# Optimization experiments

Measured on AMD Instinct MI355X. Metric: run time of the kernel, lower is better.

Reference implementation:

```python
import jax, jax.numpy as jnp
import numpy as np

N_ENT = 16384   # num_entities
N_REL = 50      # num relations
D = 128         # embedding dim
B = 4           # num bases
E = 262144      # num edges (avg degree 16)


def setup_inputs() -> dict:
    key = jax.random.key(0)
    k1, k2, k3, k4, k5, k6 = jax.random.split(key, 6)
    x = jax.random.normal(k1, (N_ENT, D), dtype=jnp.float32)
    bases = jax.random.normal(k2, (B, D, D), dtype=jnp.float32) * 0.05
    comps = jax.random.normal(k3, (N_REL, B), dtype=jnp.float32)
    alpha = jax.random.normal(k4, (N_REL, 1), dtype=jnp.float32)
    edge_index = jax.random.randint(k5, (2, E), 0, N_ENT, dtype=jnp.int64)
    edge_type = jax.random.randint(k6, (E,), 0, N_REL, dtype=jnp.int64)
    return {"x": x, "bases": bases, "comps": comps, "alpha": alpha,
            "edge_index": edge_index, "edge_type": edge_type}


def reference(x, bases, comps, alpha, edge_index, edge_type):
    # R-GCN basis-decomposition message passing:
    #   msg_e = (h_j @ W_{r(e)}) * alpha_{r(e)} * norm_e,  W_r = sum_b comps[r,b] * bases[b]
    #   out_i = sum_{e: row(e)=i} msg_e
    n = x.shape[0]
    row, col = edge_index[0], edge_index[1]

    # edge_norm = 1/sqrt(D_row) * 1/sqrt(D_col) with out-degree over rows
    ones = jnp.ones(row.shape, x.dtype)
    deg = jax.ops.segment_sum(ones, row, num_segments=n)
    deg_inv = jnp.where(deg > 0, jax.lax.rsqrt(jnp.maximum(deg, 1.0)), 0.0)
    norm = deg_inv[row] * deg_inv[col]               # [E]

    h_j = x[col]                                     # [E, D] gather
    c_e = comps[edge_type]                           # [E, B] gather
    # sum_b c[e,b] * (h_j[e] @ bases[b])  ==  einsum over (b,d)
    hj_b = c_e[:, :, None] * h_j[:, None, :]         # [E, B, D]
    msg = jnp.einsum('ebd,bdf->ef', hj_b, bases)     # [E, D] big GEMM
    msg = msg * alpha[edge_type] * norm[:, None]

    out = jax.ops.segment_sum(msg, row, num_segments=n)  # scatter-add to nodes
    return out
```

## Files before the change

kernel.cpp:

```cpp
#include <hip/hip_runtime.h>
#include <stdint.h>

#define NENT 16384
#define NREL 50
#define NE   262144
#define BSTR 64
#define ASTR 260
#define POISON 0xAAAAAAAAu

typedef __attribute__((ext_vector_type(8))) short short8;
typedef __attribute__((ext_vector_type(4))) float float4v;

__device__ __forceinline__ float bf2f(uint32_t u){ return __uint_as_float(u << 16); }
__device__ __forceinline__ uint32_t fpack(float a, float b){
  uint32_t ua = __float_as_uint(a), ub = __float_as_uint(b);
  ua = (ua + 0x7fffu + ((ua >> 16) & 1u)) >> 16;
  ub = (ub + 0x7fffu + ((ub >> 16) & 1u)) >> 16;
  return ua | (ub << 16);
}
__device__ __forceinline__ unsigned short f2bf(float a){
  uint32_t ua = __float_as_uint(a);
  return (unsigned short)((ua + 0x7fffu + ((ua >> 16) & 1u)) >> 16);
}
__device__ __forceinline__ float rdlane_f(float v, int j){
  return __uint_as_float((uint32_t)__builtin_amdgcn_readlane((int)__float_as_uint(v), j));
}

__global__ __launch_bounds__(256) void k_prep(
    const float* __restrict__ x, const float* __restrict__ W,
    const float* __restrict__ comps, const float* __restrict__ alpha,
    const int* __restrict__ eidx, const int* __restrict__ etype,
    uint32_t* __restrict__ deg, float* __restrict__ acomb,
    unsigned short* __restrict__ WTf, uint32_t* __restrict__ xbf,
    uint32_t* __restrict__ bucket)
{
  int gid = blockIdx.x * 256 + threadIdx.x;
  int row = eidx[gid], col = eidx[NE + gid], r = etype[gid];
  uint32_t pos = atomicAdd(&deg[row], 1u) - POISON;
  if (pos < BSTR) bucket[row * BSTR + pos] = (uint32_t)col | ((uint32_t)r << 14);

  const float4* xin = (const float4*)x + gid * 2;
  float4 p0 = xin[0], p1 = xin[1];
  uint32_t* xo = xbf + gid * 4;
  xo[0] = fpack(p0.x, p0.y); xo[1] = fpack(p0.z, p0.w);
  xo[2] = fpack(p1.x, p1.y); xo[3] = fpack(p1.z, p1.w);

  if (gid < 65536){
    int k = gid >> 7, c = gid & 127;
    int n = c >> 4, m = c & 15, kc = k >> 5, q = (k >> 3) & 3, jj = k & 7;
    WTf[(((n * 16 + kc) * 4 + q) * 16 + m) * 8 + jj] = f2bf(W[gid]);
  }
  if (gid < NREL * 4) acomb[gid] = alpha[gid >> 2] * comps[gid];
}

__global__ __launch_bounds__(256, 8) void k_fused(
    const uint32_t* __restrict__ xbf, const uint32_t* __restrict__ deg,
    const float* __restrict__ acomb, const uint32_t* __restrict__ bucket,
    const unsigned short* __restrict__ WTf, float* __restrict__ outf)
{
  __shared__ uint32_t A_lds[16 * ASTR];
  int t = threadIdx.x, lane = t & 63, wv = t >> 6;
  int row0 = blockIdx.x * 8;

  for (int rr = wv * 2; rr < wv * 2 + 2; ++rr){
    int i = row0 + rr;
    int d = (int)(deg[i] - POISON);
    uint32_t* Arow = &A_lds[rr * ASTR];
    if (d == 0){
      Arow[lane] = 0; Arow[lane+64] = 0; Arow[lane+128] = 0; Arow[lane+192] = 0;
      continue;
    }
    int de = min(d, BSTR);
    uint32_t rec = bucket[i * BSTR + min(lane, de - 1)];
    int colN = (int)(rec & 0x3FFFu);
    int colO = colN << 6;
    int rL   = (int)(rec >> 14);
    int dc   = (int)(deg[colN] - POISON);
    float dic = (dc > 0) ? rsqrtf((float)dc) : 0.f;
    float4 ac = make_float4(0.f, 0.f, 0.f, 0.f);
    if (lane < de){
      float4 a = ((const float4*)acomb)[rL];
      ac = make_float4(a.x * dic, a.y * dic, a.z * dic, a.w * dic);
    }
    float a0=0,a1=0,a2=0,a3=0,a4=0,a5=0,a6=0,a7=0;
    int rde = (de + 3) & ~3;
    uint32_t hA = xbf[__builtin_amdgcn_readlane(colO, 0) + lane];
    uint32_t hB = xbf[__builtin_amdgcn_readlane(colO, 1) + lane];
    uint32_t hC = xbf[__builtin_amdgcn_readlane(colO, 2) + lane];
    uint32_t hD = xbf[__builtin_amdgcn_readlane(colO, 3) + lane];
    for (int j = 0;;){
      uint32_t nA, nB, nC, nD;
      int jn = j + 4;
      if (jn < rde){
        nA = xbf[__builtin_amdgcn_readlane(colO, jn)     + lane];
        nB = xbf[__builtin_amdgcn_readlane(colO, jn + 1) + lane];
        nC = xbf[__builtin_amdgcn_readlane(colO, jn + 2) + lane];
        nD = xbf[__builtin_amdgcn_readlane(colO, jn + 3) + lane];
      }
      #define EAT(hv, e) { \
        float m0 = rdlane_f(ac.x, e), m1 = rdlane_f(ac.y, e); \
        float m2 = rdlane_f(ac.z, e), m3 = rdlane_f(ac.w, e); \
        float h0 = bf2f((hv) & 0xffffu), h1 = bf2f((hv) >> 16); \
        a0 += m0*h0; a1 += m0*h1; a2 += m1*h0; a3 += m1*h1; \
        a4 += m2*h0; a5 += m2*h1; a6 += m3*h0; a7 += m3*h1; }
      EAT(hA, j) EAT(hB, j+1) EAT(hC, j+2) EAT(hD, j+3)
      #undef EAT
      j = jn;
      if (j >= rde) break;
      hA = nA; hB = nB; hC = nC; hD = nD;
    }
    float di = rsqrtf((float)d);
    Arow[lane]       = fpack(di*a0, di*a1);
    Arow[lane + 64]  = fpack(di*a2, di*a3);
    Arow[lane + 128] = fpack(di*a4, di*a5);
    Arow[lane + 192] = fpack(di*a6, di*a7);
  }
  __syncthreads();

  int m16 = lane & 15, quad = lane >> 4;
  int n0 = wv * 2;
  const short8* Bf = (const short8*)WTf;
  const uint32_t* Abase = &A_lds[m16 * ASTR];
  float4v acc0 = {0.f,0.f,0.f,0.f}, acc1 = {0.f,0.f,0.f,0.f};
  #pragma unroll
  for (int kc = 0; kc < 16; ++kc){
    short8 aF = *(const short8*)&Abase[kc * 16 + quad * 4];
    short8 b0 = Bf[(n0 * 16 + kc) * 64 + lane];
    short8 b1 = Bf[((n0 + 1) * 16 + kc) * 64 + lane];
    acc0 = __builtin_amdgcn_mfma_f32_16x16x32_bf16(aF, b0, acc0, 0, 0, 0);
    acc1 = __builtin_amdgcn_mfma_f32_16x16x32_bf16(aF, b1, acc1, 0, 0, 0);
  }
  if (quad < 2){
    int mrow = row0 + quad * 4;
    int c0 = n0 * 16 + m16;
    #pragma unroll
    for (int r = 0; r < 4; ++r){
      outf[(mrow + r) * 128 + c0]      = acc0[r];
      outf[(mrow + r) * 128 + c0 + 16] = acc1[r];
    }
  }
}

extern "C" void kernel_launch(void* const* d_in, const int* in_sizes, int n_in,
                              void* d_out, int out_size, void* d_ws, size_t ws_size,
                              hipStream_t stream){
  (void)in_sizes; (void)n_in; (void)out_size; (void)ws_size;
  const float* x     = (const float*)d_in[0];
  const float* bases = (const float*)d_in[1];
  const float* comps = (const float*)d_in[2];
  const float* alpha = (const float*)d_in[3];
  const int* eidx    = (const int*)d_in[4];
  const int* etype   = (const int*)d_in[5];
  char* ws = (char*)d_ws;

  uint32_t* deg    = (uint32_t*) (ws + 0);
  float*    acomb  = (float*)    (ws + (64  << 10));
  unsigned short* WTf = (unsigned short*)(ws + (128 << 10));
  uint32_t* xbf    = (uint32_t*) (ws + (512 << 10));
  uint32_t* bucket = (uint32_t*) (ws + (5u  << 20));

  k_prep <<<NE / 256, 256, 0, stream>>>(x, bases, comps, alpha, eidx, etype,
                                        deg, acomb, WTf, xbf, bucket);
  k_fused<<<NENT / 8, 256, 0, stream>>>(xbf, deg, acomb, bucket, WTf,
                                        (float*)d_out);
}
```

Baseline: 106.7 us.

## Process 16 rows per block with software-pipelined bucket and feature prefetch

The fused kernel now handles 16 destination rows per block (4 per wave) instead of 8, so the MFMA tile is fully used and all 16 output rows are stored. Bucket records, degrees and the first feature gathers for upcoming rows are prefetched ahead of the current row, hiding gather latency. The per-relation coefficients are staged in LDS, and the prep kernel and output stores use nontemporal hints. In exchange it uses more registers, drops the occupancy hint from 8 to 4 blocks and launches half as many blocks. It also reads bucket entries beyond the degree, which may be stale but are masked by the lane < de check.

```diff
diff --git a/kernel.cpp b/kernel.cpp
--- a/kernel.cpp
+++ b/kernel.cpp
@@ -8,8 +8,10 @@
 #define ASTR 260
 #define POISON 0xAAAAAAAAu
 
+
 typedef __attribute__((ext_vector_type(8))) short short8;
 typedef __attribute__((ext_vector_type(4))) float float4v;
+typedef __attribute__((ext_vector_type(4))) float f32x4;
 
 __device__ __forceinline__ float bf2f(uint32_t u){ return __uint_as_float(u << 16); }
 __device__ __forceinline__ uint32_t fpack(float a, float b){
@@ -35,12 +37,15 @@
     uint32_t* __restrict__ bucket)
 {
   int gid = blockIdx.x * 256 + threadIdx.x;
-  int row = eidx[gid], col = eidx[NE + gid], r = etype[gid];
+  int row = __builtin_nontemporal_load(&eidx[gid]);
+  int col = __builtin_nontemporal_load(&eidx[NE + gid]);
+  int r   = __builtin_nontemporal_load(&etype[gid]);
   uint32_t pos = atomicAdd(&deg[row], 1u) - POISON;
   if (pos < BSTR) bucket[row * BSTR + pos] = (uint32_t)col | ((uint32_t)r << 14);
 
-  const float4* xin = (const float4*)x + gid * 2;
-  float4 p0 = xin[0], p1 = xin[1];
+  const f32x4* xin = (const f32x4*)x + gid * 2;
+  f32x4 p0 = __builtin_nontemporal_load(xin);
+  f32x4 p1 = __builtin_nontemporal_load(xin + 1);
   uint32_t* xo = xbf + gid * 4;
   xo[0] = fpack(p0.x, p0.y); xo[1] = fpack(p0.z, p0.w);
   xo[2] = fpack(p1.x, p1.y); xo[3] = fpack(p1.z, p1.w);
@@ -53,41 +58,64 @@
   if (gid < NREL * 4) acomb[gid] = alpha[gid >> 2] * comps[gid];
 }
 
-__global__ __launch_bounds__(256, 8) void k_fused(
+__global__ __launch_bounds__(256, 4) void k_fused(
     const uint32_t* __restrict__ xbf, const uint32_t* __restrict__ deg,
     const float* __restrict__ acomb, const uint32_t* __restrict__ bucket,
     const unsigned short* __restrict__ WTf, float* __restrict__ outf)
 {
   __shared__ uint32_t A_lds[16 * ASTR];
+  __shared__ float4 ac_lds[64];
   int t = threadIdx.x, lane = t & 63, wv = t >> 6;
-  int row0 = blockIdx.x * 8;
+  int row0 = blockIdx.x * 16;
 
-  for (int rr = wv * 2; rr < wv * 2 + 2; ++rr){
-    int i = row0 + rr;
-    int d = (int)(deg[i] - POISON);
-    uint32_t* Arow = &A_lds[rr * ASTR];
+  if (t < NREL) ac_lds[t] = ((const float4*)acomb)[t];
+  __syncthreads();
+
+  int ibase = row0 + wv * 4;
+  int      dS[4];
+  uint32_t recS[4];
+  int      dcS[4];
+  uint32_t h0S[4], h1S[4], h2S[4], h3S[4];
+
+  #define PRE(k) { \
+    dS[k]   = (int)(deg[ibase + (k)] - POISON); \
+    recS[k] = bucket[(ibase + (k)) * BSTR + lane]; }
+  #define MID(k) { \
+    int colN = (int)(recS[k] & 0x3FFFu); \
+    dcS[k] = (int)deg[colN]; \
+    int colO = colN << 6; \
+    h0S[k] = xbf[__builtin_amdgcn_readlane(colO, 0) + lane]; \
+    h1S[k] = xbf[__builtin_amdgcn_readlane(colO, 1) + lane]; \
+    h2S[k] = xbf[__builtin_amdgcn_readlane(colO, 2) + lane]; \
+    h3S[k] = xbf[__builtin_amdgcn_readlane(colO, 3) + lane]; }
+
+  PRE(0) PRE(1)
+  MID(0)
+  #pragma unroll
+  for (int k = 0; k < 4; ++k){
+    if (k + 2 < 4) PRE(k + 2)
+    if (k + 1 < 4) MID(k + 1)
+    int i = ibase + k;
+    int d = dS[k];
+    uint32_t* Arow = &A_lds[(wv * 4 + k) * ASTR];
     if (d == 0){
       Arow[lane] = 0; Arow[lane+64] = 0; Arow[lane+128] = 0; Arow[lane+192] = 0;
       continue;
     }
     int de = min(d, BSTR);
-    uint32_t rec = bucket[i * BSTR + min(lane, de - 1)];
-    int colN = (int)(rec & 0x3FFFu);
-    int colO = colN << 6;
-    int rL   = (int)(rec >> 14);
-    int dc   = (int)(deg[colN] - POISON);
+    uint32_t rec = recS[k];
+    int colO = (int)(rec & 0x3FFFu) << 6;
+    int rL   = (int)((rec >> 14) & 63u);
+    int dc   = dcS[k] - (int)POISON;
     float dic = (dc > 0) ? rsqrtf((float)dc) : 0.f;
     float4 ac = make_float4(0.f, 0.f, 0.f, 0.f);
     if (lane < de){
-      float4 a = ((const float4*)acomb)[rL];
+      float4 a = ac_lds[rL];
       ac = make_float4(a.x * dic, a.y * dic, a.z * dic, a.w * dic);
     }
     float a0=0,a1=0,a2=0,a3=0,a4=0,a5=0,a6=0,a7=0;
     int rde = (de + 3) & ~3;
-    uint32_t hA = xbf[__builtin_amdgcn_readlane(colO, 0) + lane];
-    uint32_t hB = xbf[__builtin_amdgcn_readlane(colO, 1) + lane];
-    uint32_t hC = xbf[__builtin_amdgcn_readlane(colO, 2) + lane];
-    uint32_t hD = xbf[__builtin_amdgcn_readlane(colO, 3) + lane];
+    uint32_t hA = h0S[k], hB = h1S[k], hC = h2S[k], hD = h3S[k];
     for (int j = 0;;){
       uint32_t nA, nB, nC, nD;
       int jn = j + 4;
@@ -115,6 +143,8 @@
     Arow[lane + 128] = fpack(di*a4, di*a5);
     Arow[lane + 192] = fpack(di*a6, di*a7);
   }
+  #undef PRE
+  #undef MID
   __syncthreads();
 
   int m16 = lane & 15, quad = lane >> 4;
@@ -130,14 +160,12 @@
     acc0 = __builtin_amdgcn_mfma_f32_16x16x32_bf16(aF, b0, acc0, 0, 0, 0);
     acc1 = __builtin_amdgcn_mfma_f32_16x16x32_bf16(aF, b1, acc1, 0, 0, 0);
   }
-  if (quad < 2){
-    int mrow = row0 + quad * 4;
-    int c0 = n0 * 16 + m16;
-    #pragma unroll
-    for (int r = 0; r < 4; ++r){
-      outf[(mrow + r) * 128 + c0]      = acc0[r];
-      outf[(mrow + r) * 128 + c0 + 16] = acc1[r];
-    }
+  int mrow = row0 + quad * 4;
+  int c0 = n0 * 16 + m16;
+  #pragma unroll
+  for (int r = 0; r < 4; ++r){
+    __builtin_nontemporal_store(acc0[r], &outf[(mrow + r) * 128 + c0]);
+    __builtin_nontemporal_store(acc1[r], &outf[(mrow + r) * 128 + c0 + 16]);
   }
 }
 
@@ -161,6 +189,6 @@
 
   k_prep <<<NE / 256, 256, 0, stream>>>(x, bases, comps, alpha, eidx, etype,
                                         deg, acomb, WTf, xbf, bucket);
-  k_fused<<<NENT / 8, 256, 0, stream>>>(xbf, deg, acomb, bucket, WTf,
-                                        (float*)d_out);
+  k_fused<<<NENT / 16, 256, 0, stream>>>(xbf, deg, acomb, bucket, WTf,
+                                         (float*)d_out);
 }
```

After: 108.0 us. Within noise of the previous version (+1.2%).

## Process two edges per wave with half-wave gathers and 16-row MFMA tiles

Applied to the files above, without the earlier changes.

The aggregation loop is restructured so each half-wave handles a different edge and each lane loads 8 bytes (4 bf16 features). The readlane-broadcast scheme with a per-wave preloaded record vector is replaced by per-iteration bucket and degree loads. Each block now covers 16 nodes instead of 8, so all 16 MFMA rows hold real data. The A tile is split into two K halves, one per half-wave partial sum, and the MFMA reduces them by accumulating both halves. This removes the wasted half-tile compute and the readlane serialization, at the cost of more LDS per block, lower occupancy bounds and redundant per-edge metadata loads.

```diff
diff --git a/kernel.cpp b/kernel.cpp
--- a/kernel.cpp
+++ b/kernel.cpp
@@ -5,8 +5,9 @@
 #define NREL 50
 #define NE   262144
 #define BSTR 64
-#define ASTR 260
+#define ASTR2 520
 #define POISON 0xAAAAAAAAu
+
 
 typedef __attribute__((ext_vector_type(8))) short short8;
 typedef __attribute__((ext_vector_type(4))) float float4v;
@@ -21,9 +22,6 @@
 __device__ __forceinline__ unsigned short f2bf(float a){
   uint32_t ua = __float_as_uint(a);
   return (unsigned short)((ua + 0x7fffu + ((ua >> 16) & 1u)) >> 16);
-}
-__device__ __forceinline__ float rdlane_f(float v, int j){
-  return __uint_as_float((uint32_t)__builtin_amdgcn_readlane((int)__float_as_uint(v), j));
 }
 
 __global__ __launch_bounds__(256) void k_prep(
@@ -53,91 +51,88 @@
   if (gid < NREL * 4) acomb[gid] = alpha[gid >> 2] * comps[gid];
 }
 
-__global__ __launch_bounds__(256, 8) void k_fused(
+__global__ __launch_bounds__(256, 4) void k_fused(
     const uint32_t* __restrict__ xbf, const uint32_t* __restrict__ deg,
     const float* __restrict__ acomb, const uint32_t* __restrict__ bucket,
     const unsigned short* __restrict__ WTf, float* __restrict__ outf)
 {
-  __shared__ uint32_t A_lds[16 * ASTR];
+  __shared__ uint32_t A_lds[16 * ASTR2];
   int t = threadIdx.x, lane = t & 63, wv = t >> 6;
-  int row0 = blockIdx.x * 8;
+  int p = lane >> 5, dl = lane & 31;
+  int row0 = blockIdx.x * 16;
+  const uint2* xb2 = (const uint2*)xbf;
+  int ubase = p * 256 + dl * 2;
 
-  for (int rr = wv * 2; rr < wv * 2 + 2; ++rr){
-    int i = row0 + rr;
+  for (int rr = 0; rr < 4; ++rr){
+    int i = row0 + wv * 4 + rr;
     int d = (int)(deg[i] - POISON);
-    uint32_t* Arow = &A_lds[rr * ASTR];
+    uint32_t* Arow = &A_lds[(wv * 4 + rr) * ASTR2];
     if (d == 0){
-      Arow[lane] = 0; Arow[lane+64] = 0; Arow[lane+128] = 0; Arow[lane+192] = 0;
+      #pragma unroll
+      for (int b = 0; b < 4; ++b){
+        Arow[ubase + b * 64] = 0; Arow[ubase + b * 64 + 1] = 0;
+      }
       continue;
     }
     int de = min(d, BSTR);
-    uint32_t rec = bucket[i * BSTR + min(lane, de - 1)];
-    int colN = (int)(rec & 0x3FFFu);
-    int colO = colN << 6;
-    int rL   = (int)(rec >> 14);
-    int dc   = (int)(deg[colN] - POISON);
-    float dic = (dc > 0) ? rsqrtf((float)dc) : 0.f;
-    float4 ac = make_float4(0.f, 0.f, 0.f, 0.f);
-    if (lane < de){
-      float4 a = ((const float4*)acomb)[rL];
-      ac = make_float4(a.x * dic, a.y * dic, a.z * dic, a.w * dic);
-    }
-    float a0=0,a1=0,a2=0,a3=0,a4=0,a5=0,a6=0,a7=0;
-    int rde = (de + 3) & ~3;
-    uint32_t hA = xbf[__builtin_amdgcn_readlane(colO, 0) + lane];
-    uint32_t hB = xbf[__builtin_amdgcn_readlane(colO, 1) + lane];
-    uint32_t hC = xbf[__builtin_amdgcn_readlane(colO, 2) + lane];
-    uint32_t hD = xbf[__builtin_amdgcn_readlane(colO, 3) + lane];
-    for (int j = 0;;){
-      uint32_t nA, nB, nC, nD;
-      int jn = j + 4;
-      if (jn < rde){
-        nA = xbf[__builtin_amdgcn_readlane(colO, jn)     + lane];
-        nB = xbf[__builtin_amdgcn_readlane(colO, jn + 1) + lane];
-        nC = xbf[__builtin_amdgcn_readlane(colO, jn + 2) + lane];
-        nD = xbf[__builtin_amdgcn_readlane(colO, jn + 3) + lane];
-      }
-      #define EAT(hv, e) { \
-        float m0 = rdlane_f(ac.x, e), m1 = rdlane_f(ac.y, e); \
-        float m2 = rdlane_f(ac.z, e), m3 = rdlane_f(ac.w, e); \
-        float h0 = bf2f((hv) & 0xffffu), h1 = bf2f((hv) >> 16); \
-        a0 += m0*h0; a1 += m0*h1; a2 += m1*h0; a3 += m1*h1; \
-        a4 += m2*h0; a5 += m2*h1; a6 += m3*h0; a7 += m3*h1; }
-      EAT(hA, j) EAT(hB, j+1) EAT(hC, j+2) EAT(hD, j+3)
-      #undef EAT
-      j = jn;
-      if (j >= rde) break;
-      hA = nA; hB = nB; hC = nC; hD = nD;
+    int nIt = (de + 1) >> 1;
+    float a00=0,a01=0,a02=0,a03=0;
+    float a10=0,a11=0,a12=0,a13=0;
+    float a20=0,a21=0,a22=0,a23=0;
+    float a30=0,a31=0,a32=0,a33=0;
+    #pragma unroll 2
+    for (int it = 0; it < nIt; ++it){
+      int slot = it * 2 + p;
+      uint32_t rec = bucket[i * BSTR + slot];
+      int colN = (int)(rec & 0x3FFFu);
+      int rL   = (int)((rec >> 14) & 63u);
+      int dc   = (int)(deg[colN] - POISON);
+      bool ok  = (slot < de) & (dc > 0);
+      float dic = ok ? rsqrtf((float)dc) : 0.f;
+      float4 aw = ((const float4*)acomb)[rL];
+      float w0 = aw.x * dic, w1 = aw.y * dic, w2 = aw.z * dic, w3 = aw.w * dic;
+      uint2 hv = xb2[(colN << 5) + dl];
+      float h0 = bf2f(hv.x & 0xffffu), h1 = bf2f(hv.x >> 16);
+      float h2 = bf2f(hv.y & 0xffffu), h3 = bf2f(hv.y >> 16);
+      a00 += w0*h0; a01 += w0*h1; a02 += w0*h2; a03 += w0*h3;
+      a10 += w1*h0; a11 += w1*h1; a12 += w1*h2; a13 += w1*h3;
+      a20 += w2*h0; a21 += w2*h1; a22 += w2*h2; a23 += w2*h3;
+      a30 += w3*h0; a31 += w3*h1; a32 += w3*h2; a33 += w3*h3;
     }
     float di = rsqrtf((float)d);
-    Arow[lane]       = fpack(di*a0, di*a1);
-    Arow[lane + 64]  = fpack(di*a2, di*a3);
-    Arow[lane + 128] = fpack(di*a4, di*a5);
-    Arow[lane + 192] = fpack(di*a6, di*a7);
+    Arow[ubase]           = fpack(di*a00, di*a01);
+    Arow[ubase + 1]       = fpack(di*a02, di*a03);
+    Arow[ubase + 64]      = fpack(di*a10, di*a11);
+    Arow[ubase + 65]      = fpack(di*a12, di*a13);
+    Arow[ubase + 128]     = fpack(di*a20, di*a21);
+    Arow[ubase + 129]     = fpack(di*a22, di*a23);
+    Arow[ubase + 192]     = fpack(di*a30, di*a31);
+    Arow[ubase + 193]     = fpack(di*a32, di*a33);
   }
   __syncthreads();
 
   int m16 = lane & 15, quad = lane >> 4;
   int n0 = wv * 2;
   const short8* Bf = (const short8*)WTf;
-  const uint32_t* Abase = &A_lds[m16 * ASTR];
+  const uint32_t* Abase = &A_lds[m16 * ASTR2];
   float4v acc0 = {0.f,0.f,0.f,0.f}, acc1 = {0.f,0.f,0.f,0.f};
   #pragma unroll
   for (int kc = 0; kc < 16; ++kc){
-    short8 aF = *(const short8*)&Abase[kc * 16 + quad * 4];
     short8 b0 = Bf[(n0 * 16 + kc) * 64 + lane];
     short8 b1 = Bf[((n0 + 1) * 16 + kc) * 64 + lane];
-    acc0 = __builtin_amdgcn_mfma_f32_16x16x32_bf16(aF, b0, acc0, 0, 0, 0);
-    acc1 = __builtin_amdgcn_mfma_f32_16x16x32_bf16(aF, b1, acc1, 0, 0, 0);
+    short8 aF0 = *(const short8*)&Abase[kc * 16 + quad * 4];
+    short8 aF1 = *(const short8*)&Abase[256 + kc * 16 + quad * 4];
+    acc0 = __builtin_amdgcn_mfma_f32_16x16x32_bf16(aF0, b0, acc0, 0, 0, 0);
+    acc1 = __builtin_amdgcn_mfma_f32_16x16x32_bf16(aF0, b1, acc1, 0, 0, 0);
+    acc0 = __builtin_amdgcn_mfma_f32_16x16x32_bf16(aF1, b0, acc0, 0, 0, 0);
+    acc1 = __builtin_amdgcn_mfma_f32_16x16x32_bf16(aF1, b1, acc1, 0, 0, 0);
   }
-  if (quad < 2){
-    int mrow = row0 + quad * 4;
-    int c0 = n0 * 16 + m16;
-    #pragma unroll
-    for (int r = 0; r < 4; ++r){
-      outf[(mrow + r) * 128 + c0]      = acc0[r];
-      outf[(mrow + r) * 128 + c0 + 16] = acc1[r];
-    }
+  int mrow = row0 + quad * 4;
+  int c0 = n0 * 16 + m16;
+  #pragma unroll
+  for (int r = 0; r < 4; ++r){
+    outf[(mrow + r) * 128 + c0]      = acc0[r];
+    outf[(mrow + r) * 128 + c0 + 16] = acc1[r];
   }
 }
 
@@ -161,6 +156,6 @@
 
   k_prep <<<NE / 256, 256, 0, stream>>>(x, bases, comps, alpha, eidx, etype,
                                         deg, acomb, WTf, xbf, bucket);
-  k_fused<<<NENT / 8, 256, 0, stream>>>(xbf, deg, acomb, bucket, WTf,
-                                        (float*)d_out);
+  k_fused<<<NENT / 16, 256, 0, stream>>>(xbf, deg, acomb, bucket, WTf,
+                                         (float*)d_out);
 }
```

After: 108.8 us. No clear change (+2.0%).
